# Optimization experiments

Hardware: AMD Instinct MI355X
Metric: run time of the kernel (lower is better)

Reference implementation:

```python
import jax, jax.numpy as jnp
import numpy as np

BUCKET_BINS = np.array([0, 1, 2, 3, 4, 5, 7, 8, 15, 16, 31, 32, 63, 64], dtype=np.int32)
MAX_WINDOW = 8  # args.span_maximum_length


def _span_index_table(L):
    # Static enumeration of all spans of width 1..MAX_WINDOW (stride-1 unfold).
    starts, ends = [], []
    for w in range(1, min(L, MAX_WINDOW) + 1):
        s = np.arange(0, L - w + 1)
        starts.append(s)
        ends.append(s + w)
    return (np.concatenate(starts).astype(np.int32),
            np.concatenate(ends).astype(np.int32))


def _bucket(width):
    # index of last bin with width >= bin value
    return jnp.searchsorted(jnp.asarray(BUCKET_BINS), width, side='right') - 1


def _fnn(h, W1, b1, W2, b2, W3, b3):
    # Linear->ReLU->(Dropout: eval identity)->Linear->ReLU->Linear->Softmax
    h = jax.nn.relu(h @ W1 + b1)
    h = jax.nn.relu(h @ W2 + b2)
    return jax.nn.softmax(h @ W3 + b3, axis=-1)


def setup_inputs() -> dict:
    key = jax.random.key(0)
    ks = jax.random.split(key, 16)
    B, L, D = 8, 256, 768
    H, WD, DD = 1024, 25, 25
    span_dim = 2 * D + WD          # 1561
    pair_dim = 2 * span_dim + DD   # 3147
    f = jnp.float32

    def g(k, shape, scale):
        return jax.random.normal(k, shape, dtype=f) * scale

    return {
        'x': g(ks[0], (B, L, D), 1.0),
        'width_emb': g(ks[1], (len(BUCKET_BINS), WD), 0.02),
        'dist_emb': g(ks[2], (len(BUCKET_BINS), DD), 0.02),
        'Ws1': g(ks[3], (span_dim, H), 0.02), 'bs1': jnp.zeros((H,), f),
        'Ws2': g(ks[4], (H, H), 0.02), 'bs2': jnp.zeros((H,), f),
        'Ws3': g(ks[5], (H, 3), 0.02), 'bs3': jnp.zeros((3,), f),
        'Wp1': g(ks[6], (pair_dim, H), 0.02), 'bp1': jnp.zeros((H,), f),
        'Wp2': g(ks[7], (H, H), 0.02), 'bp2': jnp.zeros((H,), f),
        'Wp3': g(ks[8], (H, 4), 0.02), 'bp3': jnp.zeros((4,), f),
        'nz': 64,
    }


def reference(x, width_emb, dist_emb, Ws1, bs1, Ws2, bs2, Ws3, bs3,
              Wp1, bp1, Wp2, bp2, Wp3, bp3, nz):
    B, L, D = x.shape
    starts_np, ends_np = _span_index_table(L)
    starts = jnp.asarray(starts_np)
    ends = jnp.asarray(ends_np)

    # ---- SpanRepresentation: [start token, end token, width bucket emb] ----
    w_emb = width_emb[_bucket(ends - starts)]                     # [S, WD]
    spans = jnp.concatenate([
        x[:, starts_np, :],                                       # [B,S,D]
        x[:, ends_np - 1, :],                                     # [B,S,D]
        jnp.broadcast_to(w_emb, (B,) + w_emb.shape),              # [B,S,WD]
    ], axis=-1)                                                   # [B,S,span_dim]

    # ---- span_fnn + PrunedTargetOpinion (top-k on aspect/opinion probs) ----
    span_prob = _fnn(spans, Ws1, bs1, Ws2, bs2, Ws3, bs3)         # [B,S,3]
    _, t_idx = jax.lax.top_k(span_prob[:, :, 1], nz)              # aspect  [B,nz]
    _, o_idx = jax.lax.top_k(span_prob[:, :, 2], nz)              # opinion [B,nz]

    # ---- PairRepresentation: all target x opinion pairs ----
    t_rep = jnp.take_along_axis(spans, t_idx[:, :, None], axis=1) # [B,nz,sd]
    o_rep = jnp.take_along_axis(spans, o_idx[:, :, None], axis=1)
    ta, tb = starts[t_idx], ends[t_idx]                           # [B,nz]
    oc, od = starts[o_idx], ends[o_idx]
    # min_distance(a,b,c,d) = min(|b-c|, |a-d|)
    dist = jnp.minimum(jnp.abs(tb[:, :, None] - oc[:, None, :]),
                       jnp.abs(ta[:, :, None] - od[:, None, :]))  # [B,nz,nz]
    d_emb = dist_emb[_bucket(dist)]                               # [B,nz,nz,DD]
    sd = spans.shape[-1]
    pairs = jnp.concatenate([
        jnp.broadcast_to(t_rep[:, :, None, :], (B, nz, nz, sd)),
        jnp.broadcast_to(o_rep[:, None, :, :], (B, nz, nz, sd)),
        d_emb,
    ], axis=-1).reshape(B, nz * nz, 2 * sd + d_emb.shape[-1])     # [B,nz^2,pair_dim]

    pair_prob = _fnn(pairs, Wp1, bp1, Wp2, bp2, Wp3, bp3)         # [B,nz^2,4]
    return span_prob, pair_prob
```

## Files before the change

### kernel.cpp

```cpp
#include <hip/hip_runtime.h>
#include <cstdint>
#include <cstddef>

#define BATCH 8
#define SEQ   256
#define DIM   768
#define NSPAN 2020
#define HID   1024
#define NZ    64

typedef unsigned short u16;
typedef unsigned int   u32;
typedef unsigned long long u64;

typedef __bf16 bf16x8 __attribute__((ext_vector_type(8)));
typedef float  f32x4  __attribute__((ext_vector_type(4)));

__device__ __forceinline__ u16 f2bf(float f) {
    union { float f; u32 u; } x; x.f = f;
    u32 r = x.u + 0x7fffu + ((x.u >> 16) & 1u);
    return (u16)(r >> 16);
}
__device__ __forceinline__ float bf2f(u16 b) {
    union { u32 u; float f; } x; x.u = ((u32)b) << 16;
    return x.f;
}
__device__ __forceinline__ void splitbf(float v, u16& h, u16& l) {
    h = f2bf(v);
    l = f2bf(v - bf2f(h));
}

__device__ __forceinline__ void gld_lds16(const void* g, void* l) {
    __builtin_amdgcn_global_load_lds(
        (const __attribute__((address_space(1))) unsigned int*)g,
        (__attribute__((address_space(3))) unsigned int*)l, 16, 0, 0);
}

__device__ __forceinline__ void span_decode(int s, int& start, int& end, int& w) {
    int off = 0;
#pragma unroll
    for (int wi = 1; wi <= 8; ++wi) {
        int cnt = SEQ - wi + 1;
        if (s < off + cnt) { w = wi; start = s - off; end = start + wi; return; }
        off += cnt;
    }
    w = 8; start = 0; end = 8;
}

__device__ __forceinline__ int dbucket(int d) {
    int b = 0;
    b += (d >= 1);  b += (d >= 2);  b += (d >= 3);  b += (d >= 4);
    b += (d >= 5);  b += (d >= 7);  b += (d >= 8);  b += (d >= 15);
    b += (d >= 16); b += (d >= 31); b += (d >= 32); b += (d >= 63);
    b += (d >= 64);
    return b;
}

__device__ __forceinline__ void xcd_map(int L, int sft, int& bx, int& by) {
    int grp = L >> (3 + sft);
    int rem = L & ((1 << (3 + sft)) - 1);
    bx = rem >> 3;
    by = (grp << 3) | (rem & 7);
}

__global__ __launch_bounds__(256) void k_prep(
    const float* __restrict__ x,  u16* __restrict__ xh,   u16* __restrict__ xl,
    const float* __restrict__ wemb, const float* __restrict__ demb,
    const float* __restrict__ bs1, const float* __restrict__ bp1,
    float* __restrict__ wtabS, float* __restrict__ wtabPt,
    float* __restrict__ wtabPo, float* __restrict__ dtab,
    const float* __restrict__ Ws1, u16* __restrict__ W1Th, u16* __restrict__ W1Tl,
    const float* __restrict__ Ws2, u16* __restrict__ W2Th, u16* __restrict__ W2Tl,
    const float* __restrict__ Wp2, u16* __restrict__ Wp2T,
    const float* __restrict__ Wp1, u16* __restrict__ Wp1T4)
{
    __shared__ float tile[32][33];
    const int bid = blockIdx.x, tid = threadIdx.x;
    if (bid < 6144) {
        int i = bid * 256 + tid;
        u16 h, l; splitbf(x[i], h, l);
        xh[i] = h; xl[i] = l;
        return;
    }
    if (bid < 6296) {
        int t = bid - 6144;
        int row = t >> 2;
        int h = (t & 3) * 256 + tid;
        const int wb[8] = {1,2,3,4,5,5,6,7};
        if (row < 8) {
            int bk = wb[row];
            float acc = bs1[h];
            for (int j = 0; j < 25; ++j) acc = fmaf(wemb[bk*25+j], Ws1[(size_t)(1536+j)*HID + h], acc);
            wtabS[row*HID + h] = acc;
        } else if (row < 16) {
            int bk = wb[row-8];
            float acc = 0.f;
            for (int j = 0; j < 25; ++j) acc = fmaf(wemb[bk*25+j], Wp1[(size_t)(1536+j)*HID + h], acc);
            wtabPt[(row-8)*HID + h] = acc;
        } else if (row < 24) {
            int bk = wb[row-16];
            float acc = 0.f;
            for (int j = 0; j < 25; ++j) acc = fmaf(wemb[bk*25+j], Wp1[(size_t)(3097+j)*HID + h], acc);
            wtabPo[(row-16)*HID + h] = acc;
        } else {
            int tt = row - 24;
            float acc = bp1[h];
            for (int j = 0; j < 25; ++j) acc = fmaf(demb[tt*25+j], Wp1[(size_t)(3122+j)*HID + h], acc);
            dtab[tt*HID + h] = acc;
        }
        return;
    }
    const int tb = bid - 6296;
    const int tr = tid >> 3;
    const int tc4 = (tid & 7) * 4;
    int job, tk, tn, blk = 0;
    if (tb < 1536)      { job = 0; tk = tb % 24; tn = tb / 24; }
    else if (tb < 2560) { job = 1; int t = tb - 1536; tk = t & 31; tn = t >> 5; }
    else if (tb < 3584) { job = 2; int t = tb - 2560; tk = t & 31; tn = t >> 5; }
    else                { job = 3; int t = tb - 3584; blk = t / 768; int r = t - blk * 768; tk = r % 24; tn = r / 24; }
    const int k0 = tk * 32, n0 = tn * 32;

    int k = k0 + tr;
    float4 v;
    if (job == 0) {
        const float* s = (n0 < 1024) ? (Ws1 + (size_t)k * HID + n0)
                                     : (Ws1 + (size_t)(768 + k) * HID + (n0 - 1024));
        v = *(const float4*)(s + tc4);
    } else if (job == 1) {
        v = *(const float4*)(Ws2 + (size_t)k * HID + n0 + tc4);
    } else if (job == 2) {
        v = *(const float4*)(Wp2 + (size_t)k * HID + n0 + tc4);
    } else {
        const int roff[4] = {0, 768, 1561, 2329};
        v = *(const float4*)(Wp1 + (size_t)(roff[blk] + k) * HID + n0 + tc4);
    }
    tile[tr][tc4+0] = v.x; tile[tr][tc4+1] = v.y;
    tile[tr][tc4+2] = v.z; tile[tr][tc4+3] = v.w;
    __syncthreads();

    int nn = n0 + tr;
    float w0 = tile[tc4+0][tr], w1 = tile[tc4+1][tr];
    float w2 = tile[tc4+2][tr], w3 = tile[tc4+3][tr];
    if (job == 0) {
        size_t d = (size_t)nn * 768 + k0 + tc4;
        u16 h0,l0,h1,l1,h2,l2,h3,l3;
        splitbf(w0,h0,l0); splitbf(w1,h1,l1); splitbf(w2,h2,l2); splitbf(w3,h3,l3);
        *(uint2*)(W1Th + d) = make_uint2((u32)h0 | ((u32)h1 << 16), (u32)h2 | ((u32)h3 << 16));
        *(uint2*)(W1Tl + d) = make_uint2((u32)l0 | ((u32)l1 << 16), (u32)l2 | ((u32)l3 << 16));
    } else if (job == 1) {
        size_t d = (size_t)nn * 1024 + k0 + tc4;
        u16 h0,l0,h1,l1,h2,l2,h3,l3;
        splitbf(w0,h0,l0); splitbf(w1,h1,l1); splitbf(w2,h2,l2); splitbf(w3,h3,l3);
        *(uint2*)(W2Th + d) = make_uint2((u32)h0 | ((u32)h1 << 16), (u32)h2 | ((u32)h3 << 16));
        *(uint2*)(W2Tl + d) = make_uint2((u32)l0 | ((u32)l1 << 16), (u32)l2 | ((u32)l3 << 16));
    } else if (job == 2) {
        size_t d = (size_t)nn * 1024 + k0 + tc4;
        *(uint2*)(Wp2T + d) = make_uint2((u32)f2bf(w0) | ((u32)f2bf(w1) << 16),
                                         (u32)f2bf(w2) | ((u32)f2bf(w3) << 16));
    } else {
        size_t d = (size_t)blk * 786432 + (size_t)nn * 768 + k0 + tc4;
        *(uint2*)(Wp1T4 + d) = make_uint2((u32)f2bf(w0) | ((u32)f2bf(w1) << 16),
                                          (u32)f2bf(w2) | ((u32)f2bf(w3) << 16));
    }
}

#define MFB __builtin_amdgcn_mfma_f32_16x16x32_bf16
#define MFROW(i, A, B) \
    acc[i][0] = MFB(A, B[0], acc[i][0], 0, 0, 0); \
    acc[i][1] = MFB(A, B[1], acc[i][1], 0, 0, 0); \
    acc[i][2] = MFB(A, B[2], acc[i][2], 0, 0, 0); \
    acc[i][3] = MFB(A, B[3], acc[i][3], 0, 0, 0);

__global__ __launch_bounds__(512) void k_gemm3bf(
    const u16* __restrict__ Ah, const u16* __restrict__ Al, int lda,
    const u16* __restrict__ BTh, const u16* __restrict__ BTl, int ldb,
    float* __restrict__ C, int ldc,
    int M, int K, int nby, int sft)
{
    int bx, by;
    xcd_map(blockIdx.x, sft, bx, by);
    if (by >= nby) return;
    __shared__ __align__(16) u16 sm[2 * 16384];
    const int tid = threadIdx.x;
    const int bm = by * 128, bn = bx * 128;
    const int wave = tid >> 6, lane = tid & 63;
    const int wr = wave >> 2, wc = wave & 3;
    const int q8 = lane >> 4, tl = lane & 15;

    f32x4 zero = {0.f, 0.f, 0.f, 0.f};
    f32x4 acc[4][2];
#pragma unroll
    for (int i = 0; i < 4; ++i)
#pragma unroll
        for (int j = 0; j < 2; ++j) acc[i][j] = zero;

    const int arr  = wave >> 1;
    const int half = wave & 1;
    const int sr   = lane >> 2;
    const int scs  = lane & 3;
    const int scl  = scs ^ ((sr >> 1) & 3);
    const u16* gsrc[4];
    u32 ldst[4];
#pragma unroll
    for (int j = 0; j < 4; ++j) {
        int row = ((arr < 2) ? bm : bn) + half * 64 + j * 16 + sr;
        if (arr < 2 && row >= M) row = M - 1;
        const u16* base = (arr == 0) ? Ah : (arr == 1) ? Al : (arr == 2) ? BTh : BTl;
        int ld = (arr < 2) ? lda : ldb;
        gsrc[j] = base + (size_t)row * ld + scl * 8;
        ldst[j] = arr * 4096 + half * 2048 + j * 512;
    }
    const int cpr = q8 ^ ((tl >> 1) & 3);
    const u32 lof = (u32)(tl * 32 + cpr * 8);

#pragma unroll
    for (int j = 0; j < 4; ++j) gld_lds16(gsrc[j], sm + ldst[j]);
    asm volatile("s_waitcnt vmcnt(0)" ::: "memory");
    asm volatile("s_barrier" ::: "memory");

    const int NT = K >> 5;
    for (int kt = 0; kt < NT; ++kt) {
        const u16* smr = sm + ((kt & 1) ? 16384u : 0u);
        u16*       smw = sm + ((kt & 1) ? 0u : 16384u);
        if (kt < NT - 1) {
            const int k0 = (kt + 1) * 32;
#pragma unroll
            for (int j = 0; j < 4; ++j) gld_lds16(gsrc[j] + k0, smw + ldst[j]);
            asm volatile("s_waitcnt vmcnt(4)" ::: "memory");
        } else {
            asm volatile("s_waitcnt vmcnt(0)" ::: "memory");
        }
        asm volatile("s_barrier" ::: "memory");
        __builtin_amdgcn_sched_barrier(0);
        bf16x8 ah[4], al[4], bh[2], bl[2];
#pragma unroll
        for (int fm = 0; fm < 4; ++fm) {
            ah[fm] = *(const bf16x8*)(smr + (wr*4 + fm) * 512 + lof);
            al[fm] = *(const bf16x8*)(smr + 4096 + (wr*4 + fm) * 512 + lof);
        }
#pragma unroll
        for (int fn = 0; fn < 2; ++fn) {
            bh[fn] = *(const bf16x8*)(smr + 8192 + (wc*2 + fn) * 512 + lof);
            bl[fn] = *(const bf16x8*)(smr + 12288 + (wc*2 + fn) * 512 + lof);
        }
#pragma unroll
        for (int fm = 0; fm < 4; ++fm)
#pragma unroll
            for (int fn = 0; fn < 2; ++fn) {
                acc[fm][fn] = MFB(ah[fm], bh[fn], acc[fm][fn], 0, 0, 0);
                acc[fm][fn] = MFB(al[fm], bh[fn], acc[fm][fn], 0, 0, 0);
                acc[fm][fn] = MFB(ah[fm], bl[fn], acc[fm][fn], 0, 0, 0);
            }
        asm volatile("s_barrier" ::: "memory");
    }
#pragma unroll
    for (int fm = 0; fm < 4; ++fm) {
#pragma unroll
        for (int fn = 0; fn < 2; ++fn) {
            int gcol = bn + wc*32 + fn*16 + tl;
#pragma unroll
            for (int r = 0; r < 4; ++r) {
                int grow = bm + wr*64 + fm*16 + q8*4 + r;
                if (grow >= M) continue;
                C[(size_t)grow * ldc + gcol] = acc[fm][fn][r];
            }
        }
    }
}

__global__ __launch_bounds__(512, 2) void k_span_l2(
    const u16* __restrict__ Ah, const u16* __restrict__ Al,
    const u16* __restrict__ BTh, const u16* __restrict__ BTl,
    const float* __restrict__ bs2, const float* __restrict__ Ws3,
    float* __restrict__ part, int M)
{
    __shared__ __align__(16) u16 sm[65536];
    const int tid = threadIdx.x;
    const int swz = (blockIdx.x & 7) * 32 + (blockIdx.x >> 3);
    const int by = swz >> 2, bx = swz & 3;
    const int bm = by * 256, bn = bx * 256;
    const int wave = tid >> 6, lane = tid & 63;
    const int wm = wave >> 2, wn = wave & 3;
    const int tl = lane & 15, q8 = lane >> 4;

    const int sr  = lane >> 2;
    const int scs = lane & 3;
    const int scl = scs ^ ((sr >> 1) & 3);
    const u16* gsrc[8];
    u32 ldst[8];
#pragma unroll
    for (int c = 0; c < 4; ++c) {
        int arr  = 2 + (c >> 1);
        int half = c & 1;
        int sb   = wave;
        int row  = bn + half * 128 + sb * 16 + sr;
        const u16* base = (arr == 2) ? BTh : BTl;
        gsrc[c] = base + (size_t)row * HID + scl * 8;
        ldst[c] = arr * 8192 + half * 4096 + sb * 512;
    }
#pragma unroll
    for (int p = 0; p < 4; ++p) {
        int arr  = wave >> 2;
        int half = (wave >> 1) & 1;
        int sb   = 2 * p + (wave & 1);
        int row  = bm + half * 128 + sb * 16 + sr;
        if (row >= M) row = M - 1;
        const u16* base = arr ? Al : Ah;
        gsrc[4 + p] = base + (size_t)row * HID + scl * 8;
        ldst[4 + p] = arr * 8192 + half * 4096 + sb * 512;
    }
    const int cpr = q8 ^ ((tl >> 1) & 3);
    const u32 lof = (u32)(tl * 32 + cpr * 8);
    const u32 rA  = (u32)(wm * 4096) + lof;
    const u32 rB  = 16384u + (u32)((wn >> 1) * 4096 + (wn & 1) * 2048) + lof;

    f32x4 zero = {0.f, 0.f, 0.f, 0.f};
    f32x4 acc[8][4];
#pragma unroll
    for (int i = 0; i < 8; ++i)
#pragma unroll
        for (int j = 0; j < 4; ++j) acc[i][j] = zero;

#pragma unroll
    for (int c = 0; c < 8; ++c) gld_lds16(gsrc[c], sm + ldst[c]);
    asm volatile("s_waitcnt vmcnt(3)" ::: "memory");
    asm volatile("s_barrier" ::: "memory");

    bf16x8 bh[4], bl[4];
    bf16x8 aXh0, aXh1, aXl0, aXl1, aYh0, aYh1, aYl0, aYl1;
#pragma unroll
    for (int fn = 0; fn < 4; ++fn) {
        bh[fn] = *(const bf16x8*)(sm + rB + fn * 512);
        bl[fn] = *(const bf16x8*)(sm + rB + 8192 + fn * 512);
    }
    aXh0 = *(const bf16x8*)(sm + rA + 0 * 512);
    aXh1 = *(const bf16x8*)(sm + rA + 1 * 512);
    aXl0 = *(const bf16x8*)(sm + rA + 8192 + 0 * 512);
    aXl1 = *(const bf16x8*)(sm + rA + 8192 + 1 * 512);

    for (int t = 0; t < 32; ++t) {
        const u16* smr = sm + ((t & 1) ? 32768u : 0u);
        u16*       smw = sm + ((t & 1) ? 0u : 32768u);
        const int  kn  = (t + 1) * 32;
        gld_lds16(gsrc[0] + kn, smw + ldst[0]);
        gld_lds16(gsrc[1] + kn, smw + ldst[1]);
        gld_lds16(gsrc[2] + kn, smw + ldst[2]);
        asm volatile("s_waitcnt vmcnt(5)" ::: "memory");
        asm volatile("s_barrier" ::: "memory");
        __builtin_amdgcn_sched_barrier(0);
        __builtin_amdgcn_s_setprio(1);
        MFROW(0, aXh0, bh) MFROW(1, aXh1, bh)
        MFROW(0, aXl0, bh) MFROW(1, aXl1, bh)
        MFROW(0, aXh0, bl) MFROW(1, aXh1, bl)
        __builtin_amdgcn_s_setprio(0);
        __builtin_amdgcn_sched_barrier(0);
        aYh0 = *(const bf16x8*)(smr + rA + 2 * 512);
        aYh1 = *(const bf16x8*)(smr + rA + 3 * 512);
        aYl0 = *(const bf16x8*)(smr + rA + 8192 + 2 * 512);
        aYl1 = *(const bf16x8*)(smr + rA + 8192 + 3 * 512);
        gld_lds16(gsrc[3] + kn, smw + ldst[3]);
        gld_lds16(gsrc[4] + kn, smw + ldst[4]);
        asm volatile("s_waitcnt vmcnt(6)" ::: "memory");
        asm volatile("s_barrier" ::: "memory");
        __builtin_amdgcn_sched_barrier(0);
        __builtin_amdgcn_s_setprio(1);
        MFROW(2, aYh0, bh) MFROW(3, aYh1, bh)
        MFROW(2, aYl0, bh) MFROW(3, aYl1, bh)
        MFROW(2, aYh0, bl) MFROW(3, aYh1, bl)
        __builtin_amdgcn_s_setprio(0);
        __builtin_amdgcn_sched_barrier(0);
        aXh0 = *(const bf16x8*)(smr + rA + 4 * 512);
        aXh1 = *(const bf16x8*)(smr + rA + 5 * 512);
        aXl0 = *(const bf16x8*)(smr + rA + 8192 + 4 * 512);
        aXl1 = *(const bf16x8*)(smr + rA + 8192 + 5 * 512);
        gld_lds16(gsrc[5] + kn, smw + ldst[5]);
        gld_lds16(gsrc[6] + kn, smw + ldst[6]);
        asm volatile("s_waitcnt vmcnt(7)" ::: "memory");
        asm volatile("s_barrier" ::: "memory");
        __builtin_amdgcn_sched_barrier(0);
        __builtin_amdgcn_s_setprio(1);
        MFROW(4, aXh0, bh) MFROW(5, aXh1, bh)
        MFROW(4, aXl0, bh) MFROW(5, aXl1, bh)
        MFROW(4, aXh0, bl) MFROW(5, aXh1, bl)
        __builtin_amdgcn_s_setprio(0);
        __builtin_amdgcn_sched_barrier(0);
        aYh0 = *(const bf16x8*)(smr + rA + 6 * 512);
        aYh1 = *(const bf16x8*)(smr + rA + 7 * 512);
        aYl0 = *(const bf16x8*)(smr + rA + 8192 + 6 * 512);
        aYl1 = *(const bf16x8*)(smr + rA + 8192 + 7 * 512);
        gld_lds16(gsrc[7] + kn, smw + ldst[7]);
        asm volatile("s_waitcnt vmcnt(3)" ::: "memory");
        asm volatile("s_barrier" ::: "memory");
        __builtin_amdgcn_sched_barrier(0);
        __builtin_amdgcn_s_setprio(1);
        MFROW(6, aYh0, bh) MFROW(7, aYh1, bh)
        MFROW(6, aYl0, bh) MFROW(7, aYl1, bh)
        MFROW(6, aYh0, bl) MFROW(7, aYh1, bl)
        __builtin_amdgcn_s_setprio(0);
        __builtin_amdgcn_sched_barrier(0);
        aXh0 = *(const bf16x8*)(smw + rA + 0 * 512);
        aXh1 = *(const bf16x8*)(smw + rA + 1 * 512);
        aXl0 = *(const bf16x8*)(smw + rA + 8192 + 0 * 512);
        aXl1 = *(const bf16x8*)(smw + rA + 8192 + 1 * 512);
#pragma unroll
        for (int fn = 0; fn < 4; ++fn) {
            bh[fn] = *(const bf16x8*)(smw + rB + fn * 512);
            bl[fn] = *(const bf16x8*)(smw + rB + 8192 + fn * 512);
        }
        asm volatile("s_barrier" ::: "memory");
    }

    const int slot = bx * 4 + wn;
#pragma unroll
    for (int fm = 0; fm < 8; ++fm) {
#pragma unroll
        for (int r = 0; r < 4; ++r) {
            int grow = bm + wm * 128 + fm * 16 + q8 * 4 + r;
            float l0 = 0.f, l1 = 0.f, l2 = 0.f;
#pragma unroll
            for (int fn = 0; fn < 4; ++fn) {
                int gcol = bn + wn * 64 + fn * 16 + tl;
                float v = fmaxf(acc[fm][fn][r] + bs2[gcol], 0.f);
                const float* w3 = Ws3 + gcol * 3;
                l0 = fmaf(v, w3[0], l0);
                l1 = fmaf(v, w3[1], l1);
                l2 = fmaf(v, w3[2], l2);
            }
#pragma unroll
            for (int off = 8; off > 0; off >>= 1) {
                l0 += __shfl_down(l0, off, 16);
                l1 += __shfl_down(l1, off, 16);
                l2 += __shfl_down(l2, off, 16);
            }
            if (tl == 0 && grow < M) {
                float* dst = part + ((size_t)grow * 16 + slot) * 3;
                dst[0] = l0; dst[1] = l1; dst[2] = l2;
            }
        }
    }
    asm volatile("s_waitcnt vmcnt(0)" ::: "memory");
}

__global__ __launch_bounds__(256) void k_pairL1(
    const u16* __restrict__ xh, const u16* __restrict__ Wp1T4,
    float* __restrict__ TO2, const int* __restrict__ toks)
{
    __shared__ __align__(16) u16 sm[2 * 4096];
    const int tid = threadIdx.x;
    const int bid = blockIdx.x;
    const int p = bid >> 8;
    const int bx = bid & 15, by = (bid >> 4) & 15;
    const int bm = by * 64, bn = bx * 64;
    const int wave = tid >> 6, lane = tid & 63;
    const int wr = wave >> 1, wc = wave & 1;
    const int q = lane >> 4, tl = lane & 15;
    const bool isO = bm >= 512;

    f32x4 zero = {0.f, 0.f, 0.f, 0.f};
    f32x4 acc[2][2];
#pragma unroll
    for (int i = 0; i < 2; ++i)
#pragma unroll
        for (int j = 0; j < 2; ++j) acc[i][j] = zero;

    const int srow = tid >> 2;
    const int scol = (tid & 3) * 8;
    const u32 oA = wave * 512;
    const u32 oB = 2048 + wave * 512;

    int arow = toks[bm + srow + p * 1024];
    const u16* gA = xh + (size_t)arow * DIM + scol;
    const u16* gB = Wp1T4 + ((size_t)((isO ? 2 : 0) + p) * 1024 + bn + srow) * DIM + scol;

    gld_lds16(gA, sm + oA);
    gld_lds16(gB, sm + oB);
    asm volatile("s_waitcnt vmcnt(0)" ::: "memory");
    asm volatile("s_barrier" ::: "memory");

    const int NT = DIM / 32;
    for (int kt = 0; kt < NT; ++kt) {
        const u16* smr = sm + ((kt & 1) ? 4096u : 0u);
        u16*       smw = sm + ((kt & 1) ? 0u : 4096u);
        if (kt < NT - 1) {
            const int k0 = (kt + 1) * 32;
            gld_lds16(gA + k0, smw + oA);
            gld_lds16(gB + k0, smw + oB);
            asm volatile("s_waitcnt vmcnt(2)" ::: "memory");
        } else {
            asm volatile("s_waitcnt vmcnt(0)" ::: "memory");
        }
        asm volatile("s_barrier" ::: "memory");
        bf16x8 af[2], bf[2];
#pragma unroll
        for (int t = 0; t < 2; ++t) {
            af[t] = *(const bf16x8*)(smr + (wr*32 + t*16 + tl) * 32 + q*8);
            bf[t] = *(const bf16x8*)(smr + 2048 + (wc*32 + t*16 + tl) * 32 + q*8);
        }
#pragma unroll
        for (int ti = 0; ti < 2; ++ti)
#pragma unroll
            for (int tj = 0; tj < 2; ++tj)
                acc[ti][tj] = __builtin_amdgcn_mfma_f32_16x16x32_bf16(af[ti], bf[tj], acc[ti][tj], 0, 0, 0);
        asm volatile("s_barrier" ::: "memory");
    }
    float* dstb = TO2 + (size_t)p * 1024 * HID;
#pragma unroll
    for (int ti = 0; ti < 2; ++ti) {
#pragma unroll
        for (int tj = 0; tj < 2; ++tj) {
            int gcol = bn + wc*32 + tj*16 + tl;
#pragma unroll
            for (int r = 0; r < 4; ++r) {
                int grow = bm + wr*32 + ti*16 + q*4 + r;
                dstb[(size_t)grow * HID + gcol] = acc[ti][tj][r];
            }
        }
    }
}

__global__ __launch_bounds__(256) void k_build_h1s(
    const float* __restrict__ XALL, const float* __restrict__ wtabS,
    u16* __restrict__ h1h, u16* __restrict__ h1l)
{
    int r = blockIdx.x;
    int b = r / NSPAN, s = r - b * NSPAN;
    int st, en, w; span_decode(s, st, en, w);
    const float4* xs = (const float4*)(XALL + (size_t)(b*SEQ + st) * 2048);
    const float4* xe = (const float4*)(XALL + (size_t)(b*SEQ + en - 1) * 2048 + 1024);
    const float4* wt = (const float4*)(wtabS + (size_t)(w-1) * HID);
    int t = threadIdx.x;
    float4 a = xs[t], bz = xe[t], c = wt[t];
    float v0 = fmaxf(a.x + bz.x + c.x, 0.f);
    float v1 = fmaxf(a.y + bz.y + c.y, 0.f);
    float v2 = fmaxf(a.z + bz.z + c.z, 0.f);
    float v3 = fmaxf(a.w + bz.w + c.w, 0.f);
    u16 h0,l0,h1,l1,h2,l2,h3,l3;
    splitbf(v0,h0,l0); splitbf(v1,h1,l1); splitbf(v2,h2,l2); splitbf(v3,h3,l3);
    size_t base = (size_t)r * HID + t * 4;
    *(uint2*)(h1h + base) = make_uint2((u32)h0 | ((u32)h1 << 16), (u32)h2 | ((u32)h3 << 16));
    *(uint2*)(h1l + base) = make_uint2((u32)l0 | ((u32)l1 << 16), (u32)l2 | ((u32)l3 << 16));
}

__global__ __launch_bounds__(1024) void k_topk(
    const float* __restrict__ partS, const float* __restrict__ bs3,
    float* __restrict__ out, int* __restrict__ t_idx, int* __restrict__ o_idx,
    int* __restrict__ toks)
{
    int b = blockIdx.x >> 1;
    int head = 1 + (blockIdx.x & 1);
    int* outp = (head == 1 ? t_idx : o_idx) + b * NZ;
    __shared__ u64 keys[2048];
    int tid = threadIdx.x;
#pragma unroll
    for (int ii = 0; ii < 2; ++ii) {
        int s = tid + ii * 1024;
        u32 fb = 0;
        if (s < NSPAN) {
            const float* p = partS + (size_t)(b * NSPAN + s) * 48;
            float s0 = bs3[0], s1 = bs3[1], s2 = bs3[2];
#pragma unroll
            for (int t = 0; t < 16; ++t) {
                s0 += p[t*3]; s1 += p[t*3+1]; s2 += p[t*3+2];
            }
            float m = fmaxf(s0, fmaxf(s1, s2));
            float e0 = expf(s0 - m), e1 = expf(s1 - m), e2 = expf(s2 - m);
            float inv = 1.f / (e0 + e1 + e2);
            float p0 = e0 * inv, p1 = e1 * inv, p2 = e2 * inv;
            float* o = out + (size_t)(b * NSPAN + s) * 3;
            o[0] = p0; o[1] = p1; o[2] = p2;
            union { float f; u32 u; } x;
            x.f = (head == 1) ? p1 : p2;
            fb = x.u;
        }
        keys[s] = ((u64)fb << 32) | (u64)(0xFFFFFFFFu - (u32)s);
    }
    __syncthreads();
    for (int k = 2; k <= 2048; k <<= 1) {
        for (int j = k >> 1; j > 0; j >>= 1) {
#pragma unroll
            for (int ii = 0; ii < 2; ++ii) {
                int i = tid + ii * 1024;
                int ixj = i ^ j;
                if (ixj > i) {
                    u64 a = keys[i], c = keys[ixj];
                    bool desc = (i & k) == 0;
                    bool wrong = desc ? (a < c) : (a > c);
                    if (wrong) { keys[i] = c; keys[ixj] = a; }
                }
            }
            __syncthreads();
        }
    }
    if (tid < NZ) {
        u64 key = keys[tid];
        int fi = (int)(0xFFFFFFFFu - (u32)(key & 0xFFFFFFFFu));
        if (fi < 0 || fi >= NSPAN) fi = 0;
        outp[tid] = fi;
        int st, en, w; span_decode(fi, st, en, w);
        int base = (head == 1 ? 0 : 512) + b * NZ + tid;
        toks[base] = b * SEQ + st;
        toks[1024 + base] = b * SEQ + en - 1;
    }
}

__global__ __launch_bounds__(256) void k_build_h1p(
    const float* __restrict__ TO2, const int* __restrict__ t_idx, const int* __restrict__ o_idx,
    const float* __restrict__ wtabPt, const float* __restrict__ wtabPo,
    const float* __restrict__ dtab, u16* __restrict__ h1p)
{
    __shared__ float Ts[8][HID];
    __shared__ float Os[4][HID];
    const int bid = blockIdx.x;
    const int b = bid >> 7;
    const int it = (bid >> 4) & 7;
    const int jt = bid & 15;
    const int i0 = it * 8, j0 = jt * 4;
    const int tid = threadIdx.x;
    const int k4 = tid * 4;
    const size_t PS = (size_t)1024 * HID;

    int tinfo[8][2];
    int oinfo[4][2];
#pragma unroll
    for (int r = 0; r < 8; ++r) {
        int i = i0 + r;
        int ts = t_idx[b*64 + i];
        int ta, tb, wt; span_decode(ts, ta, tb, wt);
        tinfo[r][0] = ta; tinfo[r][1] = tb;
        float4 t0 = *(const float4*)(TO2 + (size_t)(b*64 + i) * HID + k4);
        float4 t1 = *(const float4*)(TO2 + PS + (size_t)(b*64 + i) * HID + k4);
        float4 pp = *(const float4*)(wtabPt + (size_t)(wt-1) * HID + k4);
        Ts[r][k4+0] = t0.x + t1.x + pp.x;
        Ts[r][k4+1] = t0.y + t1.y + pp.y;
        Ts[r][k4+2] = t0.z + t1.z + pp.z;
        Ts[r][k4+3] = t0.w + t1.w + pp.w;
    }
#pragma unroll
    for (int r = 0; r < 4; ++r) {
        int j = j0 + r;
        int os = o_idx[b*64 + j];
        int oc, od, wo; span_decode(os, oc, od, wo);
        oinfo[r][0] = oc; oinfo[r][1] = od;
        float4 o0 = *(const float4*)(TO2 + (size_t)(512 + b*64 + j) * HID + k4);
        float4 o1 = *(const float4*)(TO2 + PS + (size_t)(512 + b*64 + j) * HID + k4);
        float4 qq = *(const float4*)(wtabPo + (size_t)(wo-1) * HID + k4);
        Os[r][k4+0] = o0.x + o1.x + qq.x;
        Os[r][k4+1] = o0.y + o1.y + qq.y;
        Os[r][k4+2] = o0.z + o1.z + qq.z;
        Os[r][k4+3] = o0.w + o1.w + qq.w;
    }
    __syncthreads();

#pragma unroll
    for (int ri = 0; ri < 8; ++ri) {
#pragma unroll
        for (int rj = 0; rj < 4; ++rj) {
            int ta = tinfo[ri][0], tb = tinfo[ri][1];
            int oc = oinfo[rj][0], od = oinfo[rj][1];
            int d1 = tb - oc; d1 = d1 < 0 ? -d1 : d1;
            int d2 = ta - od; d2 = d2 < 0 ? -d2 : d2;
            int dist = d1 < d2 ? d1 : d2;
            int db = dbucket(dist);
            const float4 dd = *(const float4*)(dtab + (size_t)db * HID + k4);
            float vx = fmaxf(Ts[ri][k4+0] + Os[rj][k4+0] + dd.x, 0.f);
            float vy = fmaxf(Ts[ri][k4+1] + Os[rj][k4+1] + dd.y, 0.f);
            float vz = fmaxf(Ts[ri][k4+2] + Os[rj][k4+2] + dd.z, 0.f);
            float vw = fmaxf(Ts[ri][k4+3] + Os[rj][k4+3] + dd.w, 0.f);
            u32 p0 = (u32)f2bf(vx) | ((u32)f2bf(vy) << 16);
            u32 p1 = (u32)f2bf(vz) | ((u32)f2bf(vw) << 16);
            int row = b * 4096 + (i0 + ri) * 64 + (j0 + rj);
            *(uint2*)(h1p + (size_t)row * HID + k4) = make_uint2(p0, p1);
        }
    }
}

#define PAIR_PHASE(P, VMC, GLDS) \
    { \
        bf16x8 a00 = *(const bf16x8*)(smr + rA + ((2*(P)+0)*2+0)*512); \
        bf16x8 a01 = *(const bf16x8*)(smr + rA + ((2*(P)+0)*2+1)*512); \
        bf16x8 a10 = *(const bf16x8*)(smr + rA + ((2*(P)+1)*2+0)*512); \
        bf16x8 a11 = *(const bf16x8*)(smr + rA + ((2*(P)+1)*2+1)*512); \
        if ((P) == 0) { \
            b0[0] = *(const bf16x8*)(smr + rB + 0*512); \
            b1[0] = *(const bf16x8*)(smr + rB + 1*512); \
            b0[1] = *(const bf16x8*)(smr + rB + 2*512); \
            b1[1] = *(const bf16x8*)(smr + rB + 3*512); \
            b0[2] = *(const bf16x8*)(smr + rB + 4*512); \
            b1[2] = *(const bf16x8*)(smr + rB + 5*512); \
            b0[3] = *(const bf16x8*)(smr + rB + 6*512); \
            b1[3] = *(const bf16x8*)(smr + rB + 7*512); \
        } \
        GLDS \
        asm volatile("s_waitcnt vmcnt(" #VMC ")" ::: "memory"); \
        asm volatile("s_barrier" ::: "memory"); \
        __builtin_amdgcn_sched_barrier(0); \
        __builtin_amdgcn_s_setprio(1); \
        MFROW(2*(P)+0, a00, b0) \
        MFROW(2*(P)+1, a10, b0) \
        MFROW(2*(P)+0, a01, b1) \
        MFROW(2*(P)+1, a11, b1) \
        __builtin_amdgcn_s_setprio(0); \
        asm volatile("s_barrier" ::: "memory"); \
    }

__global__ __launch_bounds__(512, 2) void k_pair_l2(
    const u16* __restrict__ Abf, const u16* __restrict__ BT,
    const float* __restrict__ bp2, const float* __restrict__ Wp3,
    float* __restrict__ part)
{
    __shared__ __align__(16) u16 sm[65536];
    const int tid = threadIdx.x;
    const int swz = (blockIdx.x & 7) * 64 + (blockIdx.x >> 3);
    const int by = swz >> 2, bx = swz & 3;
    const int bm = by * 256, bn = bx * 256;
    const int wave = tid >> 6, lane = tid & 63;
    const int wm = wave >> 2, wn = wave & 3;
    const int tl = lane & 15, q8 = lane >> 4;

    const int sr  = lane >> 2;
    const int scs = lane & 3;
    const int scl = scs ^ ((sr >> 1) & 3);
    const u16* gsrc[8];
    u32 ldst[8];
#pragma unroll
    for (int c = 0; c < 4; ++c) {
        int half = c >> 1;
        int sb   = (c & 1) * 8 + wave;
        int row  = bn + half * 128 + (sb >> 1) * 16 + sr;
        gsrc[c] = BT + (size_t)row * HID + (sb & 1) * 32 + scl * 8;
        ldst[c] = 16384 + half * 8192 + sb * 512;
    }
#pragma unroll
    for (int p = 0; p < 4; ++p) {
        int half = wave >> 2;
        int sb   = 4 * p + (wave & 3);
        int row  = bm + half * 128 + (sb >> 1) * 16 + sr;
        gsrc[4 + p] = Abf + (size_t)row * HID + (sb & 1) * 32 + scl * 8;
        ldst[4 + p] = half * 8192 + sb * 512;
    }
    const int cpr = q8 ^ ((tl >> 1) & 3);
    const u32 lof = (u32)(tl * 32 + cpr * 8);
    const u32 rA  = (u32)(wm * 8192) + lof;
    const u32 rB  = 16384u + (u32)((wn >> 1) * 8192 + (wn & 1) * 4096) + lof;

    f32x4 zero = {0.f, 0.f, 0.f, 0.f};
    f32x4 acc[8][4];
#pragma unroll
    for (int i = 0; i < 8; ++i)
#pragma unroll
        for (int j = 0; j < 4; ++j) acc[i][j] = zero;

#pragma unroll
    for (int c = 0; c < 8; ++c) gld_lds16(gsrc[c], sm + ldst[c]);
    asm volatile("s_waitcnt vmcnt(3)" ::: "memory");
    asm volatile("s_barrier" ::: "memory");

    bf16x8 b0[4], b1[4];
    for (int t = 0; t < 16; ++t) {
        const u16* smr = sm + ((t & 1) ? 32768u : 0u);
        u16*       smw = sm + ((t & 1) ? 0u : 32768u);
        const int  kn  = (t + 1) * 64;
        PAIR_PHASE(0, 5,
            gld_lds16(gsrc[0] + kn, smw + ldst[0]);
            gld_lds16(gsrc[1] + kn, smw + ldst[1]);
            gld_lds16(gsrc[2] + kn, smw + ldst[2]);)
        PAIR_PHASE(1, 6,
            gld_lds16(gsrc[3] + kn, smw + ldst[3]);
            gld_lds16(gsrc[4] + kn, smw + ldst[4]);)
        PAIR_PHASE(2, 7,
            gld_lds16(gsrc[5] + kn, smw + ldst[5]);
            gld_lds16(gsrc[6] + kn, smw + ldst[6]);)
        PAIR_PHASE(3, 3,
            gld_lds16(gsrc[7] + kn, smw + ldst[7]);)
    }

    const int slot = bx * 4 + wn;
#pragma unroll
    for (int fm = 0; fm < 8; ++fm) {
#pragma unroll
        for (int r = 0; r < 4; ++r) {
            int grow = bm + wm * 128 + fm * 16 + q8 * 4 + r;
            float l0 = 0.f, l1 = 0.f, l2 = 0.f, l3 = 0.f;
#pragma unroll
            for (int fn = 0; fn < 4; ++fn) {
                int gcol = bn + wn * 64 + fn * 16 + tl;
                float v = fmaxf(acc[fm][fn][r] + bp2[gcol], 0.f);
                const float4 w = *(const float4*)(Wp3 + gcol * 4);
                l0 = fmaf(v, w.x, l0); l1 = fmaf(v, w.y, l1);
                l2 = fmaf(v, w.z, l2); l3 = fmaf(v, w.w, l3);
            }
#pragma unroll
            for (int off = 8; off > 0; off >>= 1) {
                l0 += __shfl_down(l0, off, 16);
                l1 += __shfl_down(l1, off, 16);
                l2 += __shfl_down(l2, off, 16);
                l3 += __shfl_down(l3, off, 16);
            }
            if (tl == 0) {
                float* dst = part + ((size_t)grow * 16 + slot) * 4;
                dst[0] = l0; dst[1] = l1; dst[2] = l2; dst[3] = l3;
            }
        }
    }
    asm volatile("s_waitcnt vmcnt(0)" ::: "memory");
}

__global__ __launch_bounds__(256) void k_pair_red(
    const float* __restrict__ part, const float* __restrict__ bp3,
    float* __restrict__ out)
{
    int r = blockIdx.x * 256 + threadIdx.x;
    const float4* p = (const float4*)(part + (size_t)r * 64);
    float s0 = bp3[0], s1 = bp3[1], s2 = bp3[2], s3 = bp3[3];
#pragma unroll
    for (int t = 0; t < 16; ++t) {
        float4 v = p[t];
        s0 += v.x; s1 += v.y; s2 += v.z; s3 += v.w;
    }
    float m = fmaxf(fmaxf(s0, s1), fmaxf(s2, s3));
    float e0 = expf(s0 - m), e1 = expf(s1 - m), e2 = expf(s2 - m), e3 = expf(s3 - m);
    float inv = 1.f / (e0 + e1 + e2 + e3);
    float* o = out + (size_t)r * 4;
    o[0] = e0 * inv; o[1] = e1 * inv; o[2] = e2 * inv; o[3] = e3 * inv;
}

extern "C" void kernel_launch(void* const* d_in, const int* in_sizes, int n_in,
                              void* d_out, int out_size, void* d_ws, size_t ws_size,
                              hipStream_t stream)
{
    const float* x    = (const float*)d_in[0];
    const float* wemb = (const float*)d_in[1];
    const float* demb = (const float*)d_in[2];
    const float* Ws1  = (const float*)d_in[3];
    const float* bs1  = (const float*)d_in[4];
    const float* Ws2  = (const float*)d_in[5];
    const float* bs2  = (const float*)d_in[6];
    const float* Ws3  = (const float*)d_in[7];
    const float* bs3  = (const float*)d_in[8];
    const float* Wp1  = (const float*)d_in[9];
    const float* bp1  = (const float*)d_in[10];
    const float* Wp2  = (const float*)d_in[11];
    const float* bp2  = (const float*)d_in[12];
    const float* Wp3  = (const float*)d_in[13];
    const float* bp3  = (const float*)d_in[14];
    float* out = (float*)d_out;
    char* ws = (char*)d_ws;

    const size_t RSZ = (size_t)32768 * HID * 2;
    size_t off = 0;
    auto alloc = [&](size_t bytes) -> void* {
        void* p = ws + off;
        off += (bytes + 255) & ~(size_t)255;
        return p;
    };
    char* R1 = (char*)alloc(RSZ);
    char* R2 = (char*)alloc(RSZ);
    u16*   h1h  = (u16*)R1;
    u16*   h1l  = (u16*)(R1 + (size_t)16160 * HID * 2);
    float* XALL = (float*)R2;
    u16*   xl   = (u16*)(R2 + (16u << 20));
    u16*   W1Th = (u16*)(R2 + (19u << 20));
    u16*   W1Tl = (u16*)(R2 + (22u << 20));
    u16*   h1p  = (u16*)R2;
    u16*   xh     = (u16*)alloc((size_t)2048 * DIM * 2);
    float* TO2    = (float*)alloc((size_t)2 * 1024 * HID * 4);
    float* partS  = (float*)alloc((size_t)16160 * 16 * 3 * 4);
    float* partP  = (float*)alloc((size_t)32768 * 16 * 4 * 4);
    u16*   W2Th   = (u16*)alloc((size_t)1024 * 1024 * 2);
    u16*   W2Tl   = (u16*)alloc((size_t)1024 * 1024 * 2);
    u16*   Wp2T   = (u16*)alloc((size_t)1024 * 1024 * 2);
    u16*   Wp1T4  = (u16*)alloc((size_t)4 * 1024 * 768 * 2);
    float* wtabS  = (float*)alloc(8 * HID * 4);
    float* wtabPt = (float*)alloc(8 * HID * 4);
    float* wtabPo = (float*)alloc(8 * HID * 4);
    float* dtab   = (float*)alloc(14 * HID * 4);
    int*   t_idx  = (int*)alloc(BATCH * NZ * 4);
    int*   o_idx  = (int*)alloc(BATCH * NZ * 4);
    int*   toks   = (int*)alloc(2048 * 4);
    (void)ws_size; (void)in_sizes; (void)n_in; (void)out_size;

    k_prep<<<12952, 256, 0, stream>>>(x, xh, xl, wemb, demb, bs1, bp1,
                                      wtabS, wtabPt, wtabPo, dtab,
                                      Ws1, W1Th, W1Tl, Ws2, W2Th, W2Tl,
                                      Wp2, Wp2T, Wp1, Wp1T4);

    k_gemm3bf<<<256, 512, 0, stream>>>(xh, xl, 768, W1Th, W1Tl, 768,
                                       XALL, 2048, 2048, 768, 16, 4);
    k_build_h1s<<<16160, 256, 0, stream>>>(XALL, wtabS, h1h, h1l);
    k_span_l2<<<256, 512, 0, stream>>>(h1h, h1l, W2Th, W2Tl, bs2, Ws3, partS, 16160);
    k_topk<<<16, 1024, 0, stream>>>(partS, bs3, out, t_idx, o_idx, toks);
    k_pairL1<<<512, 256, 0, stream>>>(xh, Wp1T4, TO2, toks);
    k_build_h1p<<<1024, 256, 0, stream>>>(TO2, t_idx, o_idx, wtabPt, wtabPo, dtab, h1p);
    k_pair_l2<<<512, 512, 0, stream>>>(h1p, Wp2T, bp2, Wp3, partP);
    k_pair_red<<<128, 256, 0, stream>>>(partP, bp3, out + 48480);
}
```

Measured before the change: 386.9 us.

## Restructure GEMM main loops into two larger phases per k-step

Both the span layer-2 and pair layer-2 GEMM kernels move from four small compute phases per k-tile to two larger phases. Each phase loads four A fragments (plus B at the start) from LDS, issues more global-to-LDS prefetches at once, and runs 8–12 MFMAs between barriers. The A-tile load assignment is remapped so the first six prefetches cover the rows needed first, and the wait counts are adjusted to match. This cuts barrier count and gives longer MFMA bursts, but it raises register pressure and drops the cross-iteration register prefetch of fragments.

```diff
diff --git a/kernel.cpp b/kernel.cpp
--- a/kernel.cpp
+++ b/kernel.cpp
@@ -292,22 +292,21 @@
     for (int c = 0; c < 4; ++c) {
         int arr  = 2 + (c >> 1);
         int half = c & 1;
-        int sb   = wave;
-        int row  = bn + half * 128 + sb * 16 + sr;
+        int row  = bn + half * 128 + wave * 16 + sr;
         const u16* base = (arr == 2) ? BTh : BTl;
         gsrc[c] = base + (size_t)row * HID + scl * 8;
-        ldst[c] = arr * 8192 + half * 4096 + sb * 512;
-    }
-#pragma unroll
-    for (int p = 0; p < 4; ++p) {
-        int arr  = wave >> 2;
-        int half = (wave >> 1) & 1;
-        int sb   = 2 * p + (wave & 1);
+        ldst[c] = arr * 8192 + half * 4096 + wave * 512;
+    }
+#pragma unroll
+    for (int g = 0; g < 4; ++g) {
+        int arr  = g & 1;
+        int sb   = (g >> 1) * 4 + (wave & 3);
+        int half = wave >> 2;
         int row  = bm + half * 128 + sb * 16 + sr;
         if (row >= M) row = M - 1;
         const u16* base = arr ? Al : Ah;
-        gsrc[4 + p] = base + (size_t)row * HID + scl * 8;
-        ldst[4 + p] = arr * 8192 + half * 4096 + sb * 512;
+        gsrc[4 + g] = base + (size_t)row * HID + scl * 8;
+        ldst[4 + g] = arr * 8192 + half * 4096 + sb * 512;
     }
     const int cpr = q8 ^ ((tl >> 1) & 3);
     const u32 lof = (u32)(tl * 32 + cpr * 8);
@@ -323,91 +322,57 @@
 
 #pragma unroll
     for (int c = 0; c < 8; ++c) gld_lds16(gsrc[c], sm + ldst[c]);
-    asm volatile("s_waitcnt vmcnt(3)" ::: "memory");
+    asm volatile("s_waitcnt vmcnt(2)" ::: "memory");
     asm volatile("s_barrier" ::: "memory");
-
-    bf16x8 bh[4], bl[4];
-    bf16x8 aXh0, aXh1, aXl0, aXl1, aYh0, aYh1, aYl0, aYl1;
-#pragma unroll
-    for (int fn = 0; fn < 4; ++fn) {
-        bh[fn] = *(const bf16x8*)(sm + rB + fn * 512);
-        bl[fn] = *(const bf16x8*)(sm + rB + 8192 + fn * 512);
-    }
-    aXh0 = *(const bf16x8*)(sm + rA + 0 * 512);
-    aXh1 = *(const bf16x8*)(sm + rA + 1 * 512);
-    aXl0 = *(const bf16x8*)(sm + rA + 8192 + 0 * 512);
-    aXl1 = *(const bf16x8*)(sm + rA + 8192 + 1 * 512);
 
     for (int t = 0; t < 32; ++t) {
         const u16* smr = sm + ((t & 1) ? 32768u : 0u);
         u16*       smw = sm + ((t & 1) ? 0u : 32768u);
         const int  kn  = (t + 1) * 32;
-        gld_lds16(gsrc[0] + kn, smw + ldst[0]);
-        gld_lds16(gsrc[1] + kn, smw + ldst[1]);
-        gld_lds16(gsrc[2] + kn, smw + ldst[2]);
-        asm volatile("s_waitcnt vmcnt(5)" ::: "memory");
-        asm volatile("s_barrier" ::: "memory");
-        __builtin_amdgcn_sched_barrier(0);
-        __builtin_amdgcn_s_setprio(1);
-        MFROW(0, aXh0, bh) MFROW(1, aXh1, bh)
-        MFROW(0, aXl0, bh) MFROW(1, aXl1, bh)
-        MFROW(0, aXh0, bl) MFROW(1, aXh1, bl)
-        __builtin_amdgcn_s_setprio(0);
-        __builtin_amdgcn_sched_barrier(0);
-        aYh0 = *(const bf16x8*)(smr + rA + 2 * 512);
-        aYh1 = *(const bf16x8*)(smr + rA + 3 * 512);
-        aYl0 = *(const bf16x8*)(smr + rA + 8192 + 2 * 512);
-        aYl1 = *(const bf16x8*)(smr + rA + 8192 + 3 * 512);
-        gld_lds16(gsrc[3] + kn, smw + ldst[3]);
-        gld_lds16(gsrc[4] + kn, smw + ldst[4]);
-        asm volatile("s_waitcnt vmcnt(6)" ::: "memory");
-        asm volatile("s_barrier" ::: "memory");
-        __builtin_amdgcn_sched_barrier(0);
-        __builtin_amdgcn_s_setprio(1);
-        MFROW(2, aYh0, bh) MFROW(3, aYh1, bh)
-        MFROW(2, aYl0, bh) MFROW(3, aYl1, bh)
-        MFROW(2, aYh0, bl) MFROW(3, aYh1, bl)
-        __builtin_amdgcn_s_setprio(0);
-        __builtin_amdgcn_sched_barrier(0);
-        aXh0 = *(const bf16x8*)(smr + rA + 4 * 512);
-        aXh1 = *(const bf16x8*)(smr + rA + 5 * 512);
-        aXl0 = *(const bf16x8*)(smr + rA + 8192 + 4 * 512);
-        aXl1 = *(const bf16x8*)(smr + rA + 8192 + 5 * 512);
-        gld_lds16(gsrc[5] + kn, smw + ldst[5]);
-        gld_lds16(gsrc[6] + kn, smw + ldst[6]);
-        asm volatile("s_waitcnt vmcnt(7)" ::: "memory");
-        asm volatile("s_barrier" ::: "memory");
-        __builtin_amdgcn_sched_barrier(0);
-        __builtin_amdgcn_s_setprio(1);
-        MFROW(4, aXh0, bh) MFROW(5, aXh1, bh)
-        MFROW(4, aXl0, bh) MFROW(5, aXl1, bh)
-        MFROW(4, aXh0, bl) MFROW(5, aXh1, bl)
-        __builtin_amdgcn_s_setprio(0);
-        __builtin_amdgcn_sched_barrier(0);
-        aYh0 = *(const bf16x8*)(smr + rA + 6 * 512);
-        aYh1 = *(const bf16x8*)(smr + rA + 7 * 512);
-        aYl0 = *(const bf16x8*)(smr + rA + 8192 + 6 * 512);
-        aYl1 = *(const bf16x8*)(smr + rA + 8192 + 7 * 512);
-        gld_lds16(gsrc[7] + kn, smw + ldst[7]);
-        asm volatile("s_waitcnt vmcnt(3)" ::: "memory");
-        asm volatile("s_barrier" ::: "memory");
-        __builtin_amdgcn_sched_barrier(0);
-        __builtin_amdgcn_s_setprio(1);
-        MFROW(6, aYh0, bh) MFROW(7, aYh1, bh)
-        MFROW(6, aYl0, bh) MFROW(7, aYl1, bh)
-        MFROW(6, aYh0, bl) MFROW(7, aYh1, bl)
-        __builtin_amdgcn_s_setprio(0);
-        __builtin_amdgcn_sched_barrier(0);
-        aXh0 = *(const bf16x8*)(smw + rA + 0 * 512);
-        aXh1 = *(const bf16x8*)(smw + rA + 1 * 512);
-        aXl0 = *(const bf16x8*)(smw + rA + 8192 + 0 * 512);
-        aXl1 = *(const bf16x8*)(smw + rA + 8192 + 1 * 512);
-#pragma unroll
-        for (int fn = 0; fn < 4; ++fn) {
-            bh[fn] = *(const bf16x8*)(smw + rB + fn * 512);
-            bl[fn] = *(const bf16x8*)(smw + rB + 8192 + fn * 512);
-        }
-        asm volatile("s_barrier" ::: "memory");
+        bf16x8 bh[4], bl[4];
+        {
+            bf16x8 ah[4], al[4];
+#pragma unroll
+            for (int fn = 0; fn < 4; ++fn) {
+                bh[fn] = *(const bf16x8*)(smr + rB + fn * 512);
+                bl[fn] = *(const bf16x8*)(smr + rB + 8192 + fn * 512);
+            }
+#pragma unroll
+            for (int j = 0; j < 4; ++j) {
+                ah[j] = *(const bf16x8*)(smr + rA + j * 512);
+                al[j] = *(const bf16x8*)(smr + rA + 8192 + j * 512);
+            }
+#pragma unroll
+            for (int c = 0; c < 6; ++c) gld_lds16(gsrc[c] + kn, smw + ldst[c]);
+            asm volatile("s_waitcnt vmcnt(6)" ::: "memory");
+            asm volatile("s_barrier" ::: "memory");
+            __builtin_amdgcn_sched_barrier(0);
+            __builtin_amdgcn_s_setprio(1);
+            MFROW(0, ah[0], bh) MFROW(1, ah[1], bh) MFROW(2, ah[2], bh) MFROW(3, ah[3], bh)
+            MFROW(0, al[0], bh) MFROW(1, al[1], bh) MFROW(2, al[2], bh) MFROW(3, al[3], bh)
+            MFROW(0, ah[0], bl) MFROW(1, ah[1], bl) MFROW(2, ah[2], bl) MFROW(3, ah[3], bl)
+            __builtin_amdgcn_s_setprio(0);
+            asm volatile("s_barrier" ::: "memory");
+        }
+        {
+            bf16x8 ah[4], al[4];
+#pragma unroll
+            for (int j = 0; j < 4; ++j) {
+                ah[j] = *(const bf16x8*)(smr + rA + (4 + j) * 512);
+                al[j] = *(const bf16x8*)(smr + rA + 8192 + (4 + j) * 512);
+            }
+            gld_lds16(gsrc[6] + kn, smw + ldst[6]);
+            gld_lds16(gsrc[7] + kn, smw + ldst[7]);
+            asm volatile("s_waitcnt vmcnt(2)" ::: "memory");
+            asm volatile("s_barrier" ::: "memory");
+            __builtin_amdgcn_sched_barrier(0);
+            __builtin_amdgcn_s_setprio(1);
+            MFROW(4, ah[0], bh) MFROW(5, ah[1], bh) MFROW(6, ah[2], bh) MFROW(7, ah[3], bh)
+            MFROW(4, al[0], bh) MFROW(5, al[1], bh) MFROW(6, al[2], bh) MFROW(7, al[3], bh)
+            MFROW(4, ah[0], bl) MFROW(5, ah[1], bl) MFROW(6, ah[2], bl) MFROW(7, ah[3], bl)
+            __builtin_amdgcn_s_setprio(0);
+            asm volatile("s_barrier" ::: "memory");
+        }
     }
 
     const int slot = bx * 4 + wn;
@@ -674,35 +639,6 @@
     }
 }
 
-#define PAIR_PHASE(P, VMC, GLDS) \
-    { \
-        bf16x8 a00 = *(const bf16x8*)(smr + rA + ((2*(P)+0)*2+0)*512); \
-        bf16x8 a01 = *(const bf16x8*)(smr + rA + ((2*(P)+0)*2+1)*512); \
-        bf16x8 a10 = *(const bf16x8*)(smr + rA + ((2*(P)+1)*2+0)*512); \
-        bf16x8 a11 = *(const bf16x8*)(smr + rA + ((2*(P)+1)*2+1)*512); \
-        if ((P) == 0) { \
-            b0[0] = *(const bf16x8*)(smr + rB + 0*512); \
-            b1[0] = *(const bf16x8*)(smr + rB + 1*512); \
-            b0[1] = *(const bf16x8*)(smr + rB + 2*512); \
-            b1[1] = *(const bf16x8*)(smr + rB + 3*512); \
-            b0[2] = *(const bf16x8*)(smr + rB + 4*512); \
-            b1[2] = *(const bf16x8*)(smr + rB + 5*512); \
-            b0[3] = *(const bf16x8*)(smr + rB + 6*512); \
-            b1[3] = *(const bf16x8*)(smr + rB + 7*512); \
-        } \
-        GLDS \
-        asm volatile("s_waitcnt vmcnt(" #VMC ")" ::: "memory"); \
-        asm volatile("s_barrier" ::: "memory"); \
-        __builtin_amdgcn_sched_barrier(0); \
-        __builtin_amdgcn_s_setprio(1); \
-        MFROW(2*(P)+0, a00, b0) \
-        MFROW(2*(P)+1, a10, b0) \
-        MFROW(2*(P)+0, a01, b1) \
-        MFROW(2*(P)+1, a11, b1) \
-        __builtin_amdgcn_s_setprio(0); \
-        asm volatile("s_barrier" ::: "memory"); \
-    }
-
 __global__ __launch_bounds__(512, 2) void k_pair_l2(
     const u16* __restrict__ Abf, const u16* __restrict__ BT,
     const float* __restrict__ bp2, const float* __restrict__ Wp3,
@@ -731,12 +667,14 @@
         ldst[c] = 16384 + half * 8192 + sb * 512;
     }
 #pragma unroll
-    for (int p = 0; p < 4; ++p) {
-        int half = wave >> 2;
-        int sb   = 4 * p + (wave & 3);
-        int row  = bm + half * 128 + (sb >> 1) * 16 + sr;
-        gsrc[4 + p] = Abf + (size_t)row * HID + (sb & 1) * 32 + scl * 8;
-        ldst[4 + p] = half * 8192 + sb * 512;
+    for (int g = 0; g < 4; ++g) {
+        int rowsub = (g >> 1) * 4 + (wave & 3);
+        int ks     = g & 1;
+        int half   = wave >> 2;
+        int sb     = rowsub * 2 + ks;
+        int row    = bm + half * 128 + rowsub * 16 + sr;
+        gsrc[4 + g] = Abf + (size_t)row * HID + ks * 32 + scl * 8;
+        ldst[4 + g] = half * 8192 + sb * 512;
     }
     const int cpr = q8 ^ ((tl >> 1) & 3);
     const u32 lof = (u32)(tl * 32 + cpr * 8);
@@ -752,26 +690,55 @@
 
 #pragma unroll
     for (int c = 0; c < 8; ++c) gld_lds16(gsrc[c], sm + ldst[c]);
-    asm volatile("s_waitcnt vmcnt(3)" ::: "memory");
+    asm volatile("s_waitcnt vmcnt(2)" ::: "memory");
     asm volatile("s_barrier" ::: "memory");
 
-    bf16x8 b0[4], b1[4];
     for (int t = 0; t < 16; ++t) {
         const u16* smr = sm + ((t & 1) ? 32768u : 0u);
         u16*       smw = sm + ((t & 1) ? 0u : 32768u);
         const int  kn  = (t + 1) * 64;
-        PAIR_PHASE(0, 5,
-            gld_lds16(gsrc[0] + kn, smw + ldst[0]);
-            gld_lds16(gsrc[1] + kn, smw + ldst[1]);
-            gld_lds16(gsrc[2] + kn, smw + ldst[2]);)
-        PAIR_PHASE(1, 6,
-            gld_lds16(gsrc[3] + kn, smw + ldst[3]);
-            gld_lds16(gsrc[4] + kn, smw + ldst[4]);)
-        PAIR_PHASE(2, 7,
-            gld_lds16(gsrc[5] + kn, smw + ldst[5]);
-            gld_lds16(gsrc[6] + kn, smw + ldst[6]);)
-        PAIR_PHASE(3, 3,
-            gld_lds16(gsrc[7] + kn, smw + ldst[7]);)
+        bf16x8 b0[4], b1[4];
+        {
+            bf16x8 a0[4], a1[4];
+#pragma unroll
+            for (int fn = 0; fn < 4; ++fn) {
+                b0[fn] = *(const bf16x8*)(smr + rB + (fn * 2 + 0) * 512);
+                b1[fn] = *(const bf16x8*)(smr + rB + (fn * 2 + 1) * 512);
+            }
+#pragma unroll
+            for (int j = 0; j < 4; ++j) {
+                a0[j] = *(const bf16x8*)(smr + rA + (j * 2 + 0) * 512);
+                a1[j] = *(const bf16x8*)(smr + rA + (j * 2 + 1) * 512);
+            }
+#pragma unroll
+            for (int c = 0; c < 6; ++c) gld_lds16(gsrc[c] + kn, smw + ldst[c]);
+            asm volatile("s_waitcnt vmcnt(6)" ::: "memory");
+            asm volatile("s_barrier" ::: "memory");
+            __builtin_amdgcn_sched_barrier(0);
+            __builtin_amdgcn_s_setprio(1);
+            MFROW(0, a0[0], b0) MFROW(1, a0[1], b0) MFROW(2, a0[2], b0) MFROW(3, a0[3], b0)
+            MFROW(0, a1[0], b1) MFROW(1, a1[1], b1) MFROW(2, a1[2], b1) MFROW(3, a1[3], b1)
+            __builtin_amdgcn_s_setprio(0);
+            asm volatile("s_barrier" ::: "memory");
+        }
+        {
+            bf16x8 a0[4], a1[4];
+#pragma unroll
+            for (int j = 0; j < 4; ++j) {
+                a0[j] = *(const bf16x8*)(smr + rA + ((4 + j) * 2 + 0) * 512);
+                a1[j] = *(const bf16x8*)(smr + rA + ((4 + j) * 2 + 1) * 512);
+            }
+            gld_lds16(gsrc[6] + kn, smw + ldst[6]);
+            gld_lds16(gsrc[7] + kn, smw + ldst[7]);
+            asm volatile("s_waitcnt vmcnt(2)" ::: "memory");
+            asm volatile("s_barrier" ::: "memory");
+            __builtin_amdgcn_sched_barrier(0);
+            __builtin_amdgcn_s_setprio(1);
+            MFROW(4, a0[0], b0) MFROW(5, a0[1], b0) MFROW(6, a0[2], b0) MFROW(7, a0[3], b0)
+            MFROW(4, a1[0], b1) MFROW(5, a1[1], b1) MFROW(6, a1[2], b1) MFROW(7, a1[3], b1)
+            __builtin_amdgcn_s_setprio(0);
+            asm volatile("s_barrier" ::: "memory");
+        }
     }
 
     const int slot = bx * 4 + wn;
```

Result: no change. 394.3 us (+1.9%).
